# Kernel tuning notes

Measured on AMD Instinct MI355X. Metric: run time of the kernel, lower is better.

## Reference

```python
import jax, jax.numpy as jnp
import numpy as np


def _affine_grid(theta, H, W):
    # theta: [N,2,3]; matches torch affine_grid(align_corners=False)
    dt = theta.dtype
    xs = (2.0 * jnp.arange(W, dtype=dt) + 1.0) / W - 1.0
    ys = (2.0 * jnp.arange(H, dtype=dt) + 1.0) / H - 1.0
    gx, gy = jnp.meshgrid(xs, ys)          # [H,W] each, x varies along W
    coords = jnp.stack([gx, gy, jnp.ones_like(gx)], axis=-1)  # [H,W,3]
    return jnp.einsum('nij,hwj->nhwi', theta, coords)         # [N,H,W,2] (x,y)


def _gather(img, yc, xc):
    # img [N,C,H,W], yc/xc [N,Ho,Wo] int -> [N,C,Ho,Wo]
    return jax.vmap(lambda im, y, x: im[:, y, x])(img, yc, xc)


def _grid_sample(img, grid, mode):
    # torch grid_sample semantics: padding_mode='zeros', align_corners=False
    N, C, H, W = img.shape
    ix = ((grid[..., 0] + 1.0) * W - 1.0) / 2.0
    iy = ((grid[..., 1] + 1.0) * H - 1.0) / 2.0
    if mode == 'nearest':
        xr, yr = jnp.round(ix), jnp.round(iy)
        inb = ((xr >= 0) & (xr <= W - 1) & (yr >= 0) & (yr <= H - 1)).astype(img.dtype)
        xc = jnp.clip(xr, 0, W - 1).astype(jnp.int32)
        yc = jnp.clip(yr, 0, H - 1).astype(jnp.int32)
        return _gather(img, yc, xc) * inb[:, None]
    # bilinear
    x0, y0 = jnp.floor(ix), jnp.floor(iy)
    wx1, wy1 = ix - x0, iy - y0
    wx0, wy0 = 1.0 - wx1, 1.0 - wy1

    def corner(xf, yf, w):
        inb = ((xf >= 0) & (xf <= W - 1) & (yf >= 0) & (yf <= H - 1)).astype(img.dtype)
        xc = jnp.clip(xf, 0, W - 1).astype(jnp.int32)
        yc = jnp.clip(yf, 0, H - 1).astype(jnp.int32)
        return _gather(img, yc, xc) * (w * inb)[:, None]

    return (corner(x0, y0, wx0 * wy0) + corner(x0 + 1, y0, wx1 * wy0)
            + corner(x0, y0 + 1, wx0 * wy1) + corner(x0 + 1, y0 + 1, wx1 * wy1))


def _rot_theta(angles_flat):
    c, s = jnp.cos(angles_flat), jnp.sin(angles_flat)
    z = jnp.zeros_like(c)
    return jnp.stack([jnp.stack([c, -s, z], -1), jnp.stack([s, c, z], -1)], axis=1)  # [N,2,3]


def _scale_theta(scales_flat):
    z = jnp.zeros_like(scales_flat)
    return jnp.stack([jnp.stack([scales_flat, z, z], -1), jnp.stack([z, scales_flat, z], -1)], axis=1)


def setup_inputs() -> dict:
    key = jax.random.key(0)
    k1, k2, k3, k4, k5, k6 = jax.random.split(key, 6)
    B, K, C, H, W = 8, 32, 3, 128, 128
    ROT_RANGE, MIN_S, MAX_S = 0.5, 0.9, 1.1
    patches = jax.random.normal(k1, (B, K, C, H, W), dtype=jnp.float32)
    patch_labels = jax.random.uniform(k2, (B, K, 1, H, W), dtype=jnp.float32)
    angles = (jax.random.uniform(k3, (B, K), dtype=jnp.float32) * 2.0 - 1.0) * ROT_RANGE
    flip_h = jax.random.randint(k4, (B, K), 0, 2).astype(bool)
    flip_v = jax.random.randint(k5, (B, K), 0, 2).astype(bool)
    scales = MIN_S + (MAX_S - MIN_S) * jax.random.uniform(k6, (B, K), dtype=jnp.float32)
    return {"patches": patches, "patch_labels": patch_labels, "angles": angles,
            "flip_h": flip_h, "flip_v": flip_v, "scales": scales}


def reference(patches, patch_labels, angles, flip_h, flip_v, scales):
    B, K, C, H, W = patches.shape
    N = B * K
    # --- continuous rotation (same grid for image/bilinear and label/nearest) ---
    grid_r = _affine_grid(_rot_theta(angles.reshape(N)), H, W)
    p = _grid_sample(patches.reshape(N, C, H, W), grid_r, 'bilinear').reshape(B, K, C, H, W)
    l = _grid_sample(patch_labels.reshape(N, 1, H, W), grid_r, 'nearest').reshape(B, K, 1, H, W)
    # --- flips (horizontal flips W axis, vertical flips H axis) ---
    fh = flip_h[:, :, None, None, None]
    fv = flip_v[:, :, None, None, None]
    p = jnp.where(fh, p[..., ::-1], p)
    p = jnp.where(fv, p[..., ::-1, :], p)
    l = jnp.where(fh, l[..., ::-1], l)
    l = jnp.where(fv, l[..., ::-1, :], l)
    # --- scaling via affine grid ---
    grid_s = _affine_grid(_scale_theta(scales.reshape(N)), H, W)
    p = _grid_sample(p.reshape(N, C, H, W), grid_s, 'bilinear').reshape(B, K, C, H, W)
    l = _grid_sample(l.reshape(N, 1, H, W), grid_s, 'nearest').reshape(B, K, 1, H, W)
    return p, l
```

## Files before the change

kernel.cpp:

```cpp
#include <hip/hip_runtime.h>

#define HH 128
#define WW 128
#define HW (HH * WW)
#define BAND 16
#define TROWS 18


__device__ __forceinline__ float norm_coord(int i) {
    return __fsub_rn(__fmul_rn((float)(2 * i + 1), 0.0078125f), 1.0f);
}

__device__ __forceinline__ float pix_coord(float g) {
    float t = __fadd_rn(g, 1.0f);
    t = __fmul_rn(t, 128.0f);
    t = __fsub_rn(t, 1.0f);
    return __fmul_rn(t, 0.5f);
}

__device__ __forceinline__ int med127(int v) {
    return min(max(v, 0), 127);
}

__global__ void __launch_bounds__(1024, 8)
pa_all(const float* __restrict__ patches,
       const float* __restrict__ labels,
       const float* __restrict__ angles,
       const int* __restrict__ flip_h,
       const int* __restrict__ flip_v,
       const float* __restrict__ scales,
       float* __restrict__ out_p,
       float* __restrict__ out_l,
       int nlabel_blocks) {
    __shared__ float src[HW];
    __shared__ float tile[TROWS * WW];
    __shared__ float prm[5];
    int bid = blockIdx.x;
    int tid = threadIdx.x;
    bool is_label = bid < nlabel_blocks;
    int n = is_label ? bid : ((bid - nlabel_blocks) / 3);

    if (tid == 0) {
        double a = (double)angles[n];
        prm[0] = (float)cos(a);
        prm[1] = (float)sin(a);
        prm[2] = flip_h[n] ? -1.0f : 1.0f;
        prm[3] = flip_v[n] ? -1.0f : 1.0f;
        prm[4] = scales[n];
    }
    __syncthreads();
    float c = prm[0], s = prm[1], fsx = prm[2], fsy = prm[3], sc = prm[4];

    if (!is_label) {
        int slice = bid - nlabel_blocks;

        const float4* g4 = (const float4*)(patches + (size_t)slice * HW);
        float4* s4 = (float4*)src;
        #pragma unroll
        for (int i = 0; i < HW / 4 / 1024; ++i)
            s4[i * 1024 + tid] = g4[i * 1024 + tid];

        float P = c * fsx, Q = -s * fsy;
        float R = s * fsx, S = c * fsy;
        float P635 = fabsf(P) * 63.5f, R635 = fabsf(R) * 63.5f;

        int w = tid & (WW - 1);
        float wm = (float)w - 63.5f;
        int p1row = tid >> 7;

        int w2 = (tid & 63) * 2;
        int prow = tid >> 6;
        float wx0a, wx1a, wx0b, wx1b;
        int xc0a, xc1a, xc0b, xc1b;
        {
            float ixo = fmaf(sc, (float)w2 - 63.5f, 63.5f);
            float xf = floorf(ixo);
            float fx = ixo - xf;
            int xi = (int)xf;
            wx0a = ((unsigned)xi < 128u) ? (1.0f - fx) : 0.0f;
            wx1a = ((unsigned)(xi + 1) < 128u) ? fx : 0.0f;
            xc0a = med127(xi); xc1a = med127(xi + 1);
            float ixo2 = ixo + sc;
            float xf2 = floorf(ixo2);
            float fx2 = ixo2 - xf2;
            int xi2 = (int)xf2;
            wx0b = ((unsigned)xi2 < 128u) ? (1.0f - fx2) : 0.0f;
            wx1b = ((unsigned)(xi2 + 1) < 128u) ? fx2 : 0.0f;
            xc0b = med127(xi2); xc1b = med127(xi2 + 1);
        }
        __syncthreads();

        float* op = out_p + (size_t)slice * HW;

        #pragma unroll
        for (int band = 0; band < HH / BAND; ++band) {
            int r0 = band * BAND;
            float lof = floorf(fmaf(sc, (float)r0 - 63.5f, 63.5f));
            float hif = floorf(fmaf(sc, (float)(r0 + BAND - 1) - 63.5f, 63.5f)) + 1.0f;
            int lo = max((int)lof, 0);
            int hi = min((int)hif, 127);
            bool fast2 = (lof >= 0.0f) && (hif <= 127.0f);
            int nrows = hi - lo + 1;

            #pragma unroll
            for (int it = 0; it < 3; ++it) {
                int row = it * 8 + p1row;
                if (row < nrows) {
                    float hf = (float)(lo + row) - 63.5f;
                    float midx = fmaf(Q, hf, 63.5f);
                    float midy = fmaf(S, hf, 63.5f);
                    float ix = fmaf(P, wm, midx);
                    float iy = fmaf(R, wm, midy);
                    float xf = floorf(ix), yf = floorf(iy);
                    float fx = ix - xf, fy = iy - yf;
                    int xi = (int)xf, yi = (int)yf;
                    bool fast1 = (midx - P635 >= 0.25f) && (midx + P635 <= 126.75f) &&
                                 (midy - R635 >= 0.25f) && (midy + R635 <= 126.75f);
                    float o;
                    if (fast1) {
                        int b = yi * WW + xi;
                        float v00 = src[b], v10 = src[b + 1];
                        float v01 = src[b + WW], v11 = src[b + WW + 1];
                        float ra = fmaf(fx, v10 - v00, v00);
                        float rb = fmaf(fx, v11 - v01, v01);
                        o = fmaf(fy, rb - ra, ra);
                    } else {
                        float a0 = ((unsigned)xi < 128u) ? (1.0f - fx) : 0.0f;
                        float a1 = ((unsigned)(xi + 1) < 128u) ? fx : 0.0f;
                        float b0 = ((unsigned)yi < 128u) ? (1.0f - fy) : 0.0f;
                        float b1 = ((unsigned)(yi + 1) < 128u) ? fy : 0.0f;
                        int q0 = med127(xi), q1 = med127(xi + 1);
                        int p0 = med127(yi) * WW, p1 = med127(yi + 1) * WW;
                        float v00 = src[p0 + q0];
                        float v10 = src[p0 + q1];
                        float v01 = src[p1 + q0];
                        float v11 = src[p1 + q1];
                        float ra = fmaf(a1, v10, a0 * v00);
                        float rb = fmaf(a1, v11, a0 * v01);
                        o = fmaf(rb, b1, ra * b0);
                    }
                    tile[row * WW + w] = o;
                }
            }
            __syncthreads();

            {
                int h = r0 + prow;
                float iy = fmaf(sc, (float)h - 63.5f, 63.5f);
                float yf = floorf(iy);
                float fy = iy - yf;
                int yi = (int)yf;
                float ox, oy;
                if (fast2) {
                    int t0 = (yi - lo) * WW, t1 = t0 + WW;
                    float a00 = tile[t0 + xc0a], a10 = tile[t0 + xc1a];
                    float a01 = tile[t1 + xc0a], a11 = tile[t1 + xc1a];
                    float b00 = tile[t0 + xc0b], b10 = tile[t0 + xc1b];
                    float b01 = tile[t1 + xc0b], b11 = tile[t1 + xc1b];
                    float ra = fmaf(wx1a, a10, wx0a * a00);
                    float rb = fmaf(wx1a, a11, wx0a * a01);
                    ox = fmaf(fy, rb - ra, ra);
                    float rc = fmaf(wx1b, b10, wx0b * b00);
                    float rd = fmaf(wx1b, b11, wx0b * b01);
                    oy = fmaf(fy, rd - rc, rc);
                } else {
                    float wy0 = ((unsigned)yi < 128u) ? (1.0f - fy) : 0.0f;
                    float wy1 = ((unsigned)(yi + 1) < 128u) ? fy : 0.0f;
                    int t0 = (min(max(yi, lo), hi) - lo) * WW;
                    int t1 = (min(max(yi + 1, lo), hi) - lo) * WW;
                    float a00 = tile[t0 + xc0a], a10 = tile[t0 + xc1a];
                    float a01 = tile[t1 + xc0a], a11 = tile[t1 + xc1a];
                    float b00 = tile[t0 + xc0b], b10 = tile[t0 + xc1b];
                    float b01 = tile[t1 + xc0b], b11 = tile[t1 + xc1b];
                    float ra = fmaf(wx1a, a10, wx0a * a00);
                    float rb = fmaf(wx1a, a11, wx0a * a01);
                    ox = fmaf(rb, wy1, ra * wy0);
                    float rc = fmaf(wx1b, b10, wx0b * b00);
                    float rd = fmaf(wx1b, b11, wx0b * b01);
                    oy = fmaf(rd, wy1, rc * wy0);
                }
                float2 o2;
                o2.x = ox;
                o2.y = oy;
                *(float2*)&op[h * WW + w2] = o2;
            }
            __syncthreads();
        }
    } else {
        const float4* g4 = (const float4*)(labels + (size_t)n * HW);
        float4* s4 = (float4*)src;
        #pragma unroll
        for (int i = 0; i < HW / 4 / 1024; ++i)
            s4[i * 1024 + tid] = g4[i * 1024 + tid];
        __syncthreads();

        float* ol = out_l + (size_t)n * HW;
        int w = tid & (WW - 1);

        float ix2 = pix_coord(__fmul_rn(sc, norm_coord(w)));
        float xr2 = rintf(ix2);
        bool okx2 = (xr2 >= 0.0f) && (xr2 <= 127.0f);
        int w2 = (int)xr2;
        float xw2 = okx2 ? __fmul_rn(fsx, norm_coord(w2)) : 0.0f;
        float cx = __fmul_rn(c, xw2);
        float sx = __fmul_rn(s, xw2);

        #pragma unroll 4
        for (int i = 0; i < HW / 1024; ++i) {
            int p = i * 1024 + tid;
            int h = p >> 7;
            float iy2 = pix_coord(__fmul_rn(sc, norm_coord(h)));
            float yr2 = rintf(iy2);
            float outv = 0.0f;
            if (okx2 && yr2 >= 0.0f && yr2 <= 127.0f) {
                int h2 = (int)yr2;
                float y = __fmul_rn(fsy, norm_coord(h2));
                float xr1 = rintf(pix_coord(__fmaf_rn(-s, y, cx)));
                float yr1 = rintf(pix_coord(__fmaf_rn(c, y, sx)));
                if (xr1 >= 0.0f && xr1 <= 127.0f &&
                    yr1 >= 0.0f && yr1 <= 127.0f) {
                    outv = src[(int)yr1 * WW + (int)xr1];
                }
            }
            ol[p] = outv;
        }
    }
}

extern "C" void kernel_launch(void* const* d_in, const int* in_sizes, int n_in,
                              void* d_out, int out_size, void* d_ws, size_t ws_size,
                              hipStream_t stream) {
    const float* patches = (const float*)d_in[0];
    const float* labels  = (const float*)d_in[1];
    const float* angles  = (const float*)d_in[2];
    const int*   flip_h  = (const int*)d_in[3];
    const int*   flip_v  = (const int*)d_in[4];
    const float* scales  = (const float*)d_in[5];

    const int N = in_sizes[2];
    float* out   = (float*)d_out;
    float* out_p = out;
    float* out_l = out + (size_t)N * 3 * HW;

    int nlabel_blocks = N;
    int npatch_blocks = N * 3;
    pa_all<<<nlabel_blocks + npatch_blocks, 1024, 0, stream>>>(
        patches, labels, angles, flip_h, flip_v, scales,
        out_p, out_l, nlabel_blocks);
}
```

Measured before the change: 40.96 us.

## Store source image and intermediate tile in LDS as packed fp16

Source slices and the intermediate rotated tile are now kept in shared memory as packed half-precision pairs, which halves the LDS footprint so more blocks can be resident per CU. The block size drops from 1024 to 512 threads, and each thread in the rotation stage now computes two adjacent pixels. The fast-path branches for interior samples are removed. Rounding images and labels to fp16 brings precision loss, and label values that do not fit fp16 exactly would be altered, along with extra conversion instructions.

New measurement: 44.55 us. 8.8% more time.

```diff
diff --git a/kernel.cpp b/kernel.cpp
--- a/kernel.cpp
+++ b/kernel.cpp
@@ -1,4 +1,5 @@
 #include <hip/hip_runtime.h>
+#include <hip/hip_fp16.h>
 
 #define HH 128
 #define WW 128
@@ -6,23 +7,35 @@
 #define BAND 16
 #define TROWS 18
 
+typedef __fp16 h2t __attribute__((ext_vector_type(2)));
+
+__device__ __forceinline__ unsigned int pack2(float x, float y) {
+    h2t v = __builtin_amdgcn_cvt_pkrtz(x, y);
+    unsigned int u;
+    __builtin_memcpy(&u, &v, 4);
+    return u;
+}
+__device__ __forceinline__ float f16at(unsigned int u, int odd) {
+    unsigned short s = (unsigned short)(u >> (odd ? 16 : 0));
+    __half_raw hr; hr.x = s;
+    return __half2float(__half(hr));
+}
+
 
 __device__ __forceinline__ float norm_coord(int i) {
     return __fsub_rn(__fmul_rn((float)(2 * i + 1), 0.0078125f), 1.0f);
 }
-
 __device__ __forceinline__ float pix_coord(float g) {
     float t = __fadd_rn(g, 1.0f);
     t = __fmul_rn(t, 128.0f);
     t = __fsub_rn(t, 1.0f);
     return __fmul_rn(t, 0.5f);
 }
-
 __device__ __forceinline__ int med127(int v) {
     return min(max(v, 0), 127);
 }
 
-__global__ void __launch_bounds__(1024, 8)
+__global__ void __launch_bounds__(512, 8)
 pa_all(const float* __restrict__ patches,
        const float* __restrict__ labels,
        const float* __restrict__ angles,
@@ -32,8 +45,8 @@
        float* __restrict__ out_p,
        float* __restrict__ out_l,
        int nlabel_blocks) {
-    __shared__ float src[HW];
-    __shared__ float tile[TROWS * WW];
+    __shared__ unsigned int src_h[HW / 2];
+    __shared__ unsigned int tile_h[TROWS * 64];
     __shared__ float prm[5];
     int bid = blockIdx.x;
     int tid = threadIdx.x;
@@ -55,38 +68,41 @@
         int slice = bid - nlabel_blocks;
 
         const float4* g4 = (const float4*)(patches + (size_t)slice * HW);
-        float4* s4 = (float4*)src;
         #pragma unroll
-        for (int i = 0; i < HW / 4 / 1024; ++i)
-            s4[i * 1024 + tid] = g4[i * 1024 + tid];
+        for (int i = 0; i < HW / 4 / 512; ++i) {
+            int p = i * 512 + tid;
+            float4 v = g4[p];
+            src_h[2 * p]     = pack2(v.x, v.y);
+            src_h[2 * p + 1] = pack2(v.z, v.w);
+        }
 
         float P = c * fsx, Q = -s * fsy;
         float R = s * fsx, S = c * fsy;
-        float P635 = fabsf(P) * 63.5f, R635 = fabsf(R) * 63.5f;
-
-        int w = tid & (WW - 1);
-        float wm = (float)w - 63.5f;
-        int p1row = tid >> 7;
-
-        int w2 = (tid & 63) * 2;
-        int prow = tid >> 6;
+
+        int w2p = (tid & 63) * 2;
+        float wm = (float)w2p - 63.5f;
+        int rowg = tid >> 6;
+
         float wx0a, wx1a, wx0b, wx1b;
-        int xc0a, xc1a, xc0b, xc1b;
+        int xw0a, xw1a, xw0b, xw1b;
+        int pa0, pa1, pb0, pb1;
         {
-            float ixo = fmaf(sc, (float)w2 - 63.5f, 63.5f);
+            float ixo = fmaf(sc, wm, 63.5f);
             float xf = floorf(ixo);
             float fx = ixo - xf;
             int xi = (int)xf;
             wx0a = ((unsigned)xi < 128u) ? (1.0f - fx) : 0.0f;
             wx1a = ((unsigned)(xi + 1) < 128u) ? fx : 0.0f;
-            xc0a = med127(xi); xc1a = med127(xi + 1);
+            int c0 = med127(xi), c1 = med127(xi + 1);
+            xw0a = c0 >> 1; pa0 = c0 & 1; xw1a = c1 >> 1; pa1 = c1 & 1;
             float ixo2 = ixo + sc;
             float xf2 = floorf(ixo2);
             float fx2 = ixo2 - xf2;
             int xi2 = (int)xf2;
             wx0b = ((unsigned)xi2 < 128u) ? (1.0f - fx2) : 0.0f;
             wx1b = ((unsigned)(xi2 + 1) < 128u) ? fx2 : 0.0f;
-            xc0b = med127(xi2); xc1b = med127(xi2 + 1);
+            int d0 = med127(xi2), d1 = med127(xi2 + 1);
+            xw0b = d0 >> 1; pb0 = d0 & 1; xw1b = d1 >> 1; pb1 = d1 & 1;
         }
         __syncthreads();
 
@@ -99,99 +115,80 @@
             float hif = floorf(fmaf(sc, (float)(r0 + BAND - 1) - 63.5f, 63.5f)) + 1.0f;
             int lo = max((int)lof, 0);
             int hi = min((int)hif, 127);
-            bool fast2 = (lof >= 0.0f) && (hif <= 127.0f);
             int nrows = hi - lo + 1;
 
             #pragma unroll
             for (int it = 0; it < 3; ++it) {
-                int row = it * 8 + p1row;
+                int row = it * 8 + rowg;
                 if (row < nrows) {
                     float hf = (float)(lo + row) - 63.5f;
-                    float midx = fmaf(Q, hf, 63.5f);
-                    float midy = fmaf(S, hf, 63.5f);
-                    float ix = fmaf(P, wm, midx);
-                    float iy = fmaf(R, wm, midy);
-                    float xf = floorf(ix), yf = floorf(iy);
-                    float fx = ix - xf, fy = iy - yf;
-                    int xi = (int)xf, yi = (int)yf;
-                    bool fast1 = (midx - P635 >= 0.25f) && (midx + P635 <= 126.75f) &&
-                                 (midy - R635 >= 0.25f) && (midy + R635 <= 126.75f);
-                    float o;
-                    if (fast1) {
-                        int b = yi * WW + xi;
-                        float v00 = src[b], v10 = src[b + 1];
-                        float v01 = src[b + WW], v11 = src[b + WW + 1];
-                        float ra = fmaf(fx, v10 - v00, v00);
-                        float rb = fmaf(fx, v11 - v01, v01);
-                        o = fmaf(fy, rb - ra, ra);
-                    } else {
-                        float a0 = ((unsigned)xi < 128u) ? (1.0f - fx) : 0.0f;
-                        float a1 = ((unsigned)(xi + 1) < 128u) ? fx : 0.0f;
-                        float b0 = ((unsigned)yi < 128u) ? (1.0f - fy) : 0.0f;
-                        float b1 = ((unsigned)(yi + 1) < 128u) ? fy : 0.0f;
-                        int q0 = med127(xi), q1 = med127(xi + 1);
-                        int p0 = med127(yi) * WW, p1 = med127(yi + 1) * WW;
-                        float v00 = src[p0 + q0];
-                        float v10 = src[p0 + q1];
-                        float v01 = src[p1 + q0];
-                        float v11 = src[p1 + q1];
-                        float ra = fmaf(a1, v10, a0 * v00);
-                        float rb = fmaf(a1, v11, a0 * v01);
-                        o = fmaf(rb, b1, ra * b0);
+                    float ix = fmaf(P, wm, fmaf(Q, hf, 63.5f));
+                    float iy = fmaf(R, wm, fmaf(S, hf, 63.5f));
+                    float o01[2];
+                    #pragma unroll
+                    for (int px = 0; px < 2; ++px) {
+                        float xf = floorf(ix), yf = floorf(iy);
+                        float fx = ix - xf, fy = iy - yf;
+                        int xi = (int)xf, yi = (int)yf;
+                        float wx0 = ((unsigned)xi < 128u) ? (1.0f - fx) : 0.0f;
+                        float wx1 = ((unsigned)(xi + 1) < 128u) ? fx : 0.0f;
+                        float wy0 = ((unsigned)yi < 128u) ? (1.0f - fy) : 0.0f;
+                        float wy1 = ((unsigned)(yi + 1) < 128u) ? fy : 0.0f;
+                        int c0 = med127(xi), c1 = med127(xi + 1);
+                        int y0 = med127(yi) * 64, y1 = med127(yi + 1) * 64;
+                        unsigned int a0 = src_h[y0 + (c0 >> 1)];
+                        unsigned int a1 = src_h[y0 + (c1 >> 1)];
+                        unsigned int b0 = src_h[y1 + (c0 >> 1)];
+                        unsigned int b1 = src_h[y1 + (c1 >> 1)];
+                        float v00 = f16at(a0, c0 & 1), v10 = f16at(a1, c1 & 1);
+                        float v01 = f16at(b0, c0 & 1), v11 = f16at(b1, c1 & 1);
+                        float ra = fmaf(wx1, v10, wx0 * v00);
+                        float rb = fmaf(wx1, v11, wx0 * v01);
+                        o01[px] = fmaf(rb, wy1, ra * wy0);
+                        ix += P; iy += R;
                     }
-                    tile[row * WW + w] = o;
+                    tile_h[row * 64 + (tid & 63)] = pack2(o01[0], o01[1]);
                 }
             }
             __syncthreads();
 
-            {
-                int h = r0 + prow;
+            #pragma unroll
+            for (int i = 0; i < 2; ++i) {
+                int h = r0 + i * 8 + rowg;
                 float iy = fmaf(sc, (float)h - 63.5f, 63.5f);
                 float yf = floorf(iy);
                 float fy = iy - yf;
                 int yi = (int)yf;
-                float ox, oy;
-                if (fast2) {
-                    int t0 = (yi - lo) * WW, t1 = t0 + WW;
-                    float a00 = tile[t0 + xc0a], a10 = tile[t0 + xc1a];
-                    float a01 = tile[t1 + xc0a], a11 = tile[t1 + xc1a];
-                    float b00 = tile[t0 + xc0b], b10 = tile[t0 + xc1b];
-                    float b01 = tile[t1 + xc0b], b11 = tile[t1 + xc1b];
-                    float ra = fmaf(wx1a, a10, wx0a * a00);
-                    float rb = fmaf(wx1a, a11, wx0a * a01);
-                    ox = fmaf(fy, rb - ra, ra);
-                    float rc = fmaf(wx1b, b10, wx0b * b00);
-                    float rd = fmaf(wx1b, b11, wx0b * b01);
-                    oy = fmaf(fy, rd - rc, rc);
-                } else {
-                    float wy0 = ((unsigned)yi < 128u) ? (1.0f - fy) : 0.0f;
-                    float wy1 = ((unsigned)(yi + 1) < 128u) ? fy : 0.0f;
-                    int t0 = (min(max(yi, lo), hi) - lo) * WW;
-                    int t1 = (min(max(yi + 1, lo), hi) - lo) * WW;
-                    float a00 = tile[t0 + xc0a], a10 = tile[t0 + xc1a];
-                    float a01 = tile[t1 + xc0a], a11 = tile[t1 + xc1a];
-                    float b00 = tile[t0 + xc0b], b10 = tile[t0 + xc1b];
-                    float b01 = tile[t1 + xc0b], b11 = tile[t1 + xc1b];
-                    float ra = fmaf(wx1a, a10, wx0a * a00);
-                    float rb = fmaf(wx1a, a11, wx0a * a01);
-                    ox = fmaf(rb, wy1, ra * wy0);
-                    float rc = fmaf(wx1b, b10, wx0b * b00);
-                    float rd = fmaf(wx1b, b11, wx0b * b01);
-                    oy = fmaf(rd, wy1, rc * wy0);
-                }
+                float wy0 = ((unsigned)yi < 128u) ? (1.0f - fy) : 0.0f;
+                float wy1 = ((unsigned)(yi + 1) < 128u) ? fy : 0.0f;
+                int t0 = (min(max(yi, lo), hi) - lo) * 64;
+                int t1 = (min(max(yi + 1, lo), hi) - lo) * 64;
+                unsigned int ua00 = tile_h[t0 + xw0a], ua10 = tile_h[t0 + xw1a];
+                unsigned int ua01 = tile_h[t1 + xw0a], ua11 = tile_h[t1 + xw1a];
+                unsigned int ub00 = tile_h[t0 + xw0b], ub10 = tile_h[t0 + xw1b];
+                unsigned int ub01 = tile_h[t1 + xw0b], ub11 = tile_h[t1 + xw1b];
+                float ra = fmaf(wx1a, f16at(ua10, pa1), wx0a * f16at(ua00, pa0));
+                float rb = fmaf(wx1a, f16at(ua11, pa1), wx0a * f16at(ua01, pa0));
+                float ox = fmaf(rb, wy1, ra * wy0);
+                float rc = fmaf(wx1b, f16at(ub10, pb1), wx0b * f16at(ub00, pb0));
+                float rd = fmaf(wx1b, f16at(ub11, pb1), wx0b * f16at(ub01, pb0));
+                float oy = fmaf(rd, wy1, rc * wy0);
                 float2 o2;
                 o2.x = ox;
                 o2.y = oy;
-                *(float2*)&op[h * WW + w2] = o2;
+                *(float2*)&op[h * WW + w2p] = o2;
             }
             __syncthreads();
         }
     } else {
         const float4* g4 = (const float4*)(labels + (size_t)n * HW);
-        float4* s4 = (float4*)src;
         #pragma unroll
-        for (int i = 0; i < HW / 4 / 1024; ++i)
-            s4[i * 1024 + tid] = g4[i * 1024 + tid];
+        for (int i = 0; i < HW / 4 / 512; ++i) {
+            int p = i * 512 + tid;
+            float4 v = g4[p];
+            src_h[2 * p]     = pack2(v.x, v.y);
+            src_h[2 * p + 1] = pack2(v.z, v.w);
+        }
         __syncthreads();
 
         float* ol = out_l + (size_t)n * HW;
@@ -206,8 +203,8 @@
         float sx = __fmul_rn(s, xw2);
 
         #pragma unroll 4
-        for (int i = 0; i < HW / 1024; ++i) {
-            int p = i * 1024 + tid;
+        for (int i = 0; i < HW / 512; ++i) {
+            int p = i * 512 + tid;
             int h = p >> 7;
             float iy2 = pix_coord(__fmul_rn(sc, norm_coord(h)));
             float yr2 = rintf(iy2);
@@ -219,7 +216,8 @@
                 float yr1 = rintf(pix_coord(__fmaf_rn(c, y, sx)));
                 if (xr1 >= 0.0f && xr1 <= 127.0f &&
                     yr1 >= 0.0f && yr1 <= 127.0f) {
-                    outv = src[(int)yr1 * WW + (int)xr1];
+                    int idx = (int)yr1 * WW + (int)xr1;
+                    outv = f16at(src_h[idx >> 1], idx & 1);
                 }
             }
             ol[p] = outv;
@@ -244,7 +242,7 @@
 
     int nlabel_blocks = N;
     int npatch_blocks = N * 3;
-    pa_all<<<nlabel_blocks + npatch_blocks, 1024, 0, stream>>>(
+    pa_all<<<nlabel_blocks + npatch_blocks, 512, 0, stream>>>(
         patches, labels, angles, flip_h, flip_v, scales,
         out_p, out_l, nlabel_blocks);
 }
```
